# Optimization experiments

Hardware: AMD Instinct MI355X
Metric: run time of the kernel (lower is better)

The kernel has to match this reference:

```python
import jax, jax.numpy as jnp
import numpy as np

D_MODEL = 1024
N_HEADS = 16
DK = D_MODEL // N_HEADS


def setup_inputs() -> dict:
    key = jax.random.key(0)
    k1, k2, k3, k4 = jax.random.split(key, 4)
    x = jax.random.normal(k1, (2, 2048, D_MODEL), dtype=jnp.float32)
    # torch nn.Linear stores weight as [out_features, in_features]
    W_qkv = jax.random.normal(k2, (3 * D_MODEL, D_MODEL), dtype=jnp.float32) * (1.0 / np.sqrt(D_MODEL))
    W_proj = jax.random.normal(k3, (D_MODEL, D_MODEL), dtype=jnp.float32) * (1.0 / np.sqrt(D_MODEL))
    b_proj = jax.random.normal(k4, (D_MODEL,), dtype=jnp.float32) * 0.01
    return {"x": x, "W_qkv": W_qkv, "W_proj": W_proj, "b_proj": b_proj}


def reference(x, W_qkv, W_proj, b_proj):
    B, L, D = x.shape
    qkv = x @ W_qkv.T                      # [B, L, 3D]
    q, k, v = jnp.split(qkv, 3, axis=-1)   # each [B, L, D]

    def split_heads(t):
        return t.reshape(B, L, N_HEADS, DK).transpose(0, 2, 1, 3)  # [B, H, L, dk]

    q, k, v = map(split_heads, (q, k, v))
    scale = jnp.float32(1.0 / np.sqrt(DK))
    scores = jnp.einsum('bhid,bhjd->bhij', q, k) * scale  # [B, H, L, L]
    attn = jax.nn.softmax(scores, axis=-1)
    out = jnp.einsum('bhij,bhjd->bhid', attn, v)           # [B, H, L, dk]
    out = out.transpose(0, 2, 1, 3).reshape(B, L, D)
    return out @ W_proj.T + b_proj
```

## Files before the change

kernel.cpp:

```cpp
#include <hip/hip_runtime.h>
#include <stdint.h>

typedef unsigned short ushort_t;
typedef __bf16 bf16x4 __attribute__((ext_vector_type(4)));
typedef __bf16 bf16x8 __attribute__((ext_vector_type(8)));
typedef float f32x4 __attribute__((ext_vector_type(4)));
typedef float f32x16 __attribute__((ext_vector_type(16)));
typedef unsigned short us8 __attribute__((ext_vector_type(8)));
typedef unsigned short us4v __attribute__((ext_vector_type(4)));

__device__ __forceinline__ float bf2f(ushort_t u) {
  union { uint32_t u; float f; } v; v.u = ((uint32_t)u) << 16; return v.f;
}
__device__ __forceinline__ ushort_t f2bf(float f) {
  union { float f; uint32_t u; } v; v.f = f;
  uint32_t u = v.u;
  uint32_t r = (u + 0x7FFFu + ((u >> 16) & 1u)) >> 16;
  return (ushort_t)r;
}
__device__ __forceinline__ uint32_t pkbf(float a, float b) {
  __bf16 x = (__bf16)a, y = (__bf16)b;
  uint32_t ux = __builtin_bit_cast(unsigned short, x);
  uint32_t uy = __builtin_bit_cast(unsigned short, y);
  return ux | (uy << 16);
}
__device__ __forceinline__ void gload_lds16(const void* g, void* l) {
  __builtin_amdgcn_global_load_lds(
      (const __attribute__((address_space(1))) void*)g,
      (__attribute__((address_space(3))) void*)l, 16, 0, 0);
}
__device__ __forceinline__ void tr2(const ushort_t* p, bf16x4& lo, bf16x4& hi) {
  asm volatile("ds_read_b64_tr_b16 %0, %2\n\t"
               "ds_read_b64_tr_b16 %1, %2 offset:128"
               : "=&v"(lo), "=&v"(hi)
               : "v"((const __attribute__((address_space(3))) ushort_t*)p));
}

template <typename T> __device__ __forceinline__ T to_out(float f);
template <> __device__ __forceinline__ ushort_t to_out<ushort_t>(float f) { return f2bf(f); }
template <> __device__ __forceinline__ float to_out<float>(float f) { return f; }

__global__ void f2b_kernel(const float* __restrict__ in, ushort_t* __restrict__ out, int n4) {
  int i = blockIdx.x * blockDim.x + threadIdx.x;
  int stride = gridDim.x * blockDim.x;
  for (; i < n4; i += stride) {
    float4 v = ((const float4*)in)[i];
    us4v o;
    o[0] = f2bf(v.x); o[1] = f2bf(v.y); o[2] = f2bf(v.z); o[3] = f2bf(v.w);
    ((us4v*)out)[i] = o;
  }
}

template<bool BIAS, typename OT>
__global__ __launch_bounds__(256, 2) void gemm_bt(
    const ushort_t* __restrict__ A, const ushort_t* __restrict__ W,
    const float* __restrict__ bias, OT* __restrict__ C,
    int M, int N, int K)
{
  __shared__ ushort_t As[128 * 64];
  __shared__ ushort_t Bs[128 * 64];
  const int t = threadIdx.x;
  const int w = t >> 6, lane = t & 63;
  const int lg = lane >> 4, lc = lane & 15;
  const int rowbase = blockIdx.y * 128;
  const int colbase = blockIdx.x * 128;
  const int wr = (w >> 1) * 64, wc = (w & 1) * 64;

  f32x4 acc[4][4] = {};
  const int nkt = K >> 6;

  for (int kt = 0; kt < nkt; ++kt) {
#pragma unroll
    for (int i = 0; i < 4; ++i) {
      int off = (i * 256 + t) * 16;
      int row = off >> 7;
      int cb  = off & 127;
      int ec  = cb ^ ((row & 7) << 4);
      gload_lds16(A + (size_t)(rowbase + row) * K + kt * 64 + (ec >> 1),
                  (char*)As + off);
      gload_lds16(W + (size_t)(colbase + row) * K + kt * 64 + (ec >> 1),
                  (char*)Bs + off);
    }
    __syncthreads();
#pragma unroll
    for (int kk = 0; kk < 2; ++kk) {
      bf16x8 af[4], bf[4];
#pragma unroll
      for (int m = 0; m < 4; ++m) {
        int row = wr + m * 16 + lc;
        int kb  = (lg * 16 + kk * 64) ^ ((row & 7) << 4);
        af[m] = *(const bf16x8*)((const char*)As + row * 128 + kb);
        int col = wc + m * 16 + lc;
        int kb2 = (lg * 16 + kk * 64) ^ ((col & 7) << 4);
        bf[m] = *(const bf16x8*)((const char*)Bs + col * 128 + kb2);
      }
#pragma unroll
      for (int m = 0; m < 4; ++m)
#pragma unroll
        for (int n = 0; n < 4; ++n)
          acc[m][n] = __builtin_amdgcn_mfma_f32_16x16x32_bf16(af[m], bf[n],
                                                              acc[m][n], 0, 0, 0);
    }
    __syncthreads();
  }

#pragma unroll
  for (int m = 0; m < 4; ++m) {
    int r0 = rowbase + wr + m * 16 + lg * 4;
#pragma unroll
    for (int n = 0; n < 4; ++n) {
      int c0 = colbase + wc + n * 16 + lc;
      float bv = 0.f;
      if (BIAS) bv = bias[c0];
#pragma unroll
      for (int j = 0; j < 4; ++j)
        C[(size_t)(r0 + j) * N + c0] = to_out<OT>(acc[m][n][j] + bv);
    }
  }
}

__global__ __launch_bounds__(256, 2) void attn_fwd(
    const ushort_t* __restrict__ qkv, ushort_t* __restrict__ aout)
{
  __shared__ ushort_t Ks[2][64 * 64];
  __shared__ ushort_t Vs[2][64 * 64];

  const int t = threadIdx.x, w = t >> 6, lane = t & 63;
  const int l31 = lane & 31, hi = lane >> 5;
  const int lc = lane & 15;

  const int d = blockIdx.x;
  const int qt = (d >> 3) & 15;
  const int bh = (d & 7) * 4 + (d >> 7);
  const int b = bh >> 4, h = bh & 15;

  const ushort_t* Qg = qkv + (size_t)(b * 2048) * 3072 + h * 64;
  const ushort_t* Kg = Qg + 1024;
  const ushort_t* Vg = Qg + 2048;

  auto stage_k = [&](ushort_t* Kd, int kt) {
#pragma unroll
    for (int i = 0; i < 2; ++i) {
      int off = (i * 256 + t) * 16;
      int row = off >> 7;
      int cb  = off & 127;
      int ec  = cb ^ ((row & 7) << 4);
      gload_lds16(Kg + (size_t)(kt * 64 + row) * 3072 + (ec >> 1),
                  (char*)Kd + off);
    }
  };
  int vr[2], vc0[2], vdst[2];
#pragma unroll
  for (int i = 0; i < 2; ++i) {
    int u = i * 256 + t;
    vr[i]  = u >> 3;
    vc0[i] = (u & 7) * 8;
    vdst[i] = (vc0[i] >> 4) * 2048 + (vr[i] >> 2) * 128 + (vr[i] & 3) * 32 +
              (vc0[i] & 8) * 2;
  }

  const ushort_t* qrow_p = Qg + (size_t)(qt * 128 + w * 32 + l31) * 3072;
  bf16x8 qf[4];
#pragma unroll
  for (int kk = 0; kk < 4; ++kk)
    qf[kk] = *(const bf16x8*)(qrow_p + kk * 16 + hi * 8);

  stage_k(Ks[0], 0);
#pragma unroll
  for (int i = 0; i < 2; ++i) {
    us8 v = *(const us8*)(Vg + (size_t)vr[i] * 3072 + vc0[i]);
    *(us8*)((char*)Vs[0] + vdst[i]) = v;
  }
  __syncthreads();

  f32x16 oacc0 = {}, oacc1 = {};
  float m = -1e30f, l = 0.f;
  const float SC = 0.125f * 1.44269504088896f;

  int cur = 0;
  for (int kt = 0; kt < 32; ++kt) {
    us8 vnext[2];
    if (kt < 31) {
      stage_k(Ks[cur ^ 1], kt + 1);
#pragma unroll
      for (int i = 0; i < 2; ++i)
        vnext[i] = *(const us8*)(Vg + (size_t)((kt + 1) * 64 + vr[i]) * 3072 + vc0[i]);
    }

    const ushort_t* Kc = Ks[cur];
    f32x16 s0 = {}, s1 = {};
#pragma unroll
    for (int kk = 0; kk < 4; ++kk) {
      int cbyte = (kk * 32 + hi * 16);
      int r0 = l31, r1 = 32 + l31;
      bf16x8 kf0 = *(const bf16x8*)((const char*)Kc + r0 * 128 +
                                    (cbyte ^ ((r0 & 7) << 4)));
      bf16x8 kf1 = *(const bf16x8*)((const char*)Kc + r1 * 128 +
                                    (cbyte ^ ((r1 & 7) << 4)));
      s0 = __builtin_amdgcn_mfma_f32_32x32x16_bf16(kf0, qf[kk], s0, 0, 0, 0);
      s1 = __builtin_amdgcn_mfma_f32_32x32x16_bf16(kf1, qf[kk], s1, 0, 0, 0);
    }

    float tm = fmaxf(s0[0], s1[0]);
#pragma unroll
    for (int i = 1; i < 16; ++i) tm = fmaxf(tm, fmaxf(s0[i], s1[i]));
    tm = fmaxf(tm, __shfl_xor(tm, 32));
    float tms = tm * SC;
    if (__any(tms > m + 8.f)) {
      float nm = fmaxf(m, tms);
      float so = __builtin_amdgcn_exp2f(m - nm);
      m = nm; l *= so;
#pragma unroll
      for (int r = 0; r < 16; ++r) {
        float sor = __shfl(so, (r & 3) + 8 * (r >> 2) + 4 * hi);
        oacc0[r] *= sor; oacc1[r] *= sor;
      }
    }
#pragma unroll
    for (int i = 0; i < 16; ++i) {
      s0[i] = __builtin_amdgcn_exp2f(__builtin_fmaf(s0[i], SC, -m));
      s1[i] = __builtin_amdgcn_exp2f(__builtin_fmaf(s1[i], SC, -m));
    }
    float rs = 0.f;
#pragma unroll
    for (int i = 0; i < 16; ++i) rs += s0[i] + s1[i];
    rs += __shfl_xor(rs, 32);
    l += rs;

    uint32_t pk0[8], pk1[8];
#pragma unroll
    for (int j = 0; j < 8; ++j) {
      pk0[j] = pkbf(s0[2 * j], s0[2 * j + 1]);
      pk1[j] = pkbf(s1[2 * j], s1[2 * j + 1]);
    }

    if (kt < 31) {
#pragma unroll
      for (int i = 0; i < 2; ++i)
        *(us8*)((char*)Vs[cur ^ 1] + vdst[i]) = vnext[i];
    }

    const ushort_t* Vc = Vs[cur];
    bf16x8 pa[4], vf[4][2];
#pragma unroll
    for (int ks = 0; ks < 4; ++ks) {
      int j0 = 4 * (ks & 1);
      uint32_t x0 = (ks < 2) ? pk0[j0]     : pk1[j0];
      uint32_t x1 = (ks < 2) ? pk0[j0 + 1] : pk1[j0 + 1];
      uint32_t y0 = (ks < 2) ? pk0[j0 + 2] : pk1[j0 + 2];
      uint32_t y1 = (ks < 2) ? pk0[j0 + 3] : pk1[j0 + 3];
      asm volatile("v_permlane32_swap_b32 %0, %1" : "+v"(x0), "+v"(y0));
      asm volatile("v_permlane32_swap_b32 %0, %1" : "+v"(x1), "+v"(y1));
      union { uint32_t du[4]; bf16x8 v; } U;
      U.du[0] = x0; U.du[1] = x1; U.du[2] = y0; U.du[3] = y1;
      pa[ks] = U.v;
      const int m16 = (lane >> 4) & 1;
#pragma unroll
      for (int nd = 0; nd < 2; ++nd) {
        bf16x4 lo, hh;
        tr2(Vc + (nd * 2 + m16) * 1024 + (4 * ks + 2 * hi) * 64 + lc * 4, lo, hh);
        vf[ks][nd] = __builtin_shufflevector(lo, hh, 0, 1, 2, 3, 4, 5, 6, 7);
      }
    }
    asm volatile("s_waitcnt lgkmcnt(0)" ::: "memory");
    __builtin_amdgcn_sched_barrier(0);
#pragma unroll
    for (int ks = 0; ks < 4; ++ks) {
      oacc0 = __builtin_amdgcn_mfma_f32_32x32x16_bf16(pa[ks], vf[ks][0], oacc0, 0, 0, 0);
      oacc1 = __builtin_amdgcn_mfma_f32_32x32x16_bf16(pa[ks], vf[ks][1], oacc1, 0, 0, 0);
    }

    __syncthreads();
    cur ^= 1;
  }

  float inv = 1.f / l;
#pragma unroll
  for (int r = 0; r < 16; ++r) {
    int crow = (r & 3) + 8 * (r >> 2) + 4 * hi;
    float iq = __shfl(inv, crow);
    int qrow = qt * 128 + w * 32 + crow;
    size_t base = ((size_t)(b * 2048 + qrow)) * 1024 + h * 64 + l31;
    aout[base]      = f2bf(oacc0[r] * iq);
    aout[base + 32] = f2bf(oacc1[r] * iq);
  }
}

extern "C" void kernel_launch(void* const* d_in, const int* in_sizes, int n_in,
                              void* d_out, int out_size, void* d_ws, size_t ws_size,
                              hipStream_t stream) {
  const float* x     = (const float*)d_in[0];
  const float* Wqkv  = (const float*)d_in[1];
  const float* Wproj = (const float*)d_in[2];
  const float* bproj = (const float*)d_in[3];
  float* out = (float*)d_out;

  ushort_t* qkv   = (ushort_t*)d_ws;
  ushort_t* aout  = qkv   + (size_t)4096 * 3072;
  ushort_t* xb    = aout  + (size_t)4096 * 1024;
  ushort_t* wqb   = xb    + (size_t)4096 * 1024;
  ushort_t* wpb   = wqb   + (size_t)3072 * 1024;

  dim3 blk(256);
  f2b_kernel<<<1024, blk, 0, stream>>>(x,     xb,  4096 * 1024 / 4);
  f2b_kernel<<<1024, blk, 0, stream>>>(Wqkv,  wqb, 3072 * 1024 / 4);
  f2b_kernel<<<512,  blk, 0, stream>>>(Wproj, wpb, 1024 * 1024 / 4);

  gemm_bt<false, ushort_t><<<dim3(24, 32), blk, 0, stream>>>(
      xb, wqb, nullptr, qkv, 4096, 3072, 1024);
  attn_fwd<<<dim3(512), blk, 0, stream>>>(qkv, aout);
  gemm_bt<true, float><<<dim3(8, 32), blk, 0, stream>>>(
      aout, wpb, bproj, out, 4096, 1024, 1024);
}
```

Baseline: 125.7 us.

## Load K tiles directly into registers instead of staging through LDS

Each wave now loads its K fragments straight from global memory into double-buffered register arrays (kA/kB) and prefetches the next tile, rather than staging K through swizzled shared memory with async LDS loads. The loop is unrolled by two so the K and V buffers alternate without an index variable, and the max reduction is rewritten as a linear chain. This removes the LDS traffic and LDS footprint for K. In exchange, each of the four waves fetches the same K rows from global memory or cache, and the extra 16 bf16x8 registers may push up register pressure under the 2-blocks-per-CU launch bound.

```diff
diff --git a/kernel.cpp b/kernel.cpp
--- a/kernel.cpp
+++ b/kernel.cpp
@@ -122,7 +122,6 @@
 __global__ __launch_bounds__(256, 2) void attn_fwd(
     const ushort_t* __restrict__ qkv, ushort_t* __restrict__ aout)
 {
-  __shared__ ushort_t Ks[2][64 * 64];
   __shared__ ushort_t Vs[2][64 * 64];
 
   const int t = threadIdx.x, w = t >> 6, lane = t & 63;
@@ -138,17 +137,6 @@
   const ushort_t* Kg = Qg + 1024;
   const ushort_t* Vg = Qg + 2048;
 
-  auto stage_k = [&](ushort_t* Kd, int kt) {
-#pragma unroll
-    for (int i = 0; i < 2; ++i) {
-      int off = (i * 256 + t) * 16;
-      int row = off >> 7;
-      int cb  = off & 127;
-      int ec  = cb ^ ((row & 7) << 4);
-      gload_lds16(Kg + (size_t)(kt * 64 + row) * 3072 + (ec >> 1),
-                  (char*)Kd + off);
-    }
-  };
   int vr[2], vc0[2], vdst[2];
 #pragma unroll
   for (int i = 0; i < 2; ++i) {
@@ -165,7 +153,15 @@
   for (int kk = 0; kk < 4; ++kk)
     qf[kk] = *(const bf16x8*)(qrow_p + kk * 16 + hi * 8);
 
-  stage_k(Ks[0], 0);
+  const ushort_t* krow0 = Kg + (size_t)l31 * 3072 + hi * 8;
+  const ushort_t* krow1 = Kg + (size_t)(32 + l31) * 3072 + hi * 8;
+
+  bf16x8 kA[8], kB[8];
+#pragma unroll
+  for (int kk = 0; kk < 4; ++kk) {
+    kA[2 * kk]     = *(const bf16x8*)(krow0 + kk * 16);
+    kA[2 * kk + 1] = *(const bf16x8*)(krow1 + kk * 16);
+  }
 #pragma unroll
   for (int i = 0; i < 2; ++i) {
     us8 v = *(const us8*)(Vg + (size_t)vr[i] * 3072 + vc0[i]);
@@ -176,103 +172,118 @@
   f32x16 oacc0 = {}, oacc1 = {};
   float m = -1e30f, l = 0.f;
   const float SC = 0.125f * 1.44269504088896f;
-
-  int cur = 0;
-  for (int kt = 0; kt < 32; ++kt) {
-    us8 vnext[2];
-    if (kt < 31) {
-      stage_k(Ks[cur ^ 1], kt + 1);
-#pragma unroll
-      for (int i = 0; i < 2; ++i)
-        vnext[i] = *(const us8*)(Vg + (size_t)((kt + 1) * 64 + vr[i]) * 3072 + vc0[i]);
-    }
-
-    const ushort_t* Kc = Ks[cur];
-    f32x16 s0 = {}, s1 = {};
-#pragma unroll
-    for (int kk = 0; kk < 4; ++kk) {
-      int cbyte = (kk * 32 + hi * 16);
-      int r0 = l31, r1 = 32 + l31;
-      bf16x8 kf0 = *(const bf16x8*)((const char*)Kc + r0 * 128 +
-                                    (cbyte ^ ((r0 & 7) << 4)));
-      bf16x8 kf1 = *(const bf16x8*)((const char*)Kc + r1 * 128 +
-                                    (cbyte ^ ((r1 & 7) << 4)));
-      s0 = __builtin_amdgcn_mfma_f32_32x32x16_bf16(kf0, qf[kk], s0, 0, 0, 0);
-      s1 = __builtin_amdgcn_mfma_f32_32x32x16_bf16(kf1, qf[kk], s1, 0, 0, 0);
-    }
-
-    float tm = fmaxf(s0[0], s1[0]);
-#pragma unroll
-    for (int i = 1; i < 16; ++i) tm = fmaxf(tm, fmaxf(s0[i], s1[i]));
-    tm = fmaxf(tm, __shfl_xor(tm, 32));
-    float tms = tm * SC;
-    if (__any(tms > m + 8.f)) {
-      float nm = fmaxf(m, tms);
-      float so = __builtin_amdgcn_exp2f(m - nm);
-      m = nm; l *= so;
-#pragma unroll
-      for (int r = 0; r < 16; ++r) {
-        float sor = __shfl(so, (r & 3) + 8 * (r >> 2) + 4 * hi);
-        oacc0[r] *= sor; oacc1[r] *= sor;
-      }
-    }
-#pragma unroll
-    for (int i = 0; i < 16; ++i) {
-      s0[i] = __builtin_amdgcn_exp2f(__builtin_fmaf(s0[i], SC, -m));
-      s1[i] = __builtin_amdgcn_exp2f(__builtin_fmaf(s1[i], SC, -m));
-    }
-    float rs = 0.f;
-#pragma unroll
-    for (int i = 0; i < 16; ++i) rs += s0[i] + s1[i];
-    rs += __shfl_xor(rs, 32);
-    l += rs;
-
-    uint32_t pk0[8], pk1[8];
-#pragma unroll
-    for (int j = 0; j < 8; ++j) {
-      pk0[j] = pkbf(s0[2 * j], s0[2 * j + 1]);
-      pk1[j] = pkbf(s1[2 * j], s1[2 * j + 1]);
-    }
-
-    if (kt < 31) {
-#pragma unroll
-      for (int i = 0; i < 2; ++i)
-        *(us8*)((char*)Vs[cur ^ 1] + vdst[i]) = vnext[i];
-    }
-
-    const ushort_t* Vc = Vs[cur];
-    bf16x8 pa[4], vf[4][2];
-#pragma unroll
-    for (int ks = 0; ks < 4; ++ks) {
-      int j0 = 4 * (ks & 1);
-      uint32_t x0 = (ks < 2) ? pk0[j0]     : pk1[j0];
-      uint32_t x1 = (ks < 2) ? pk0[j0 + 1] : pk1[j0 + 1];
-      uint32_t y0 = (ks < 2) ? pk0[j0 + 2] : pk1[j0 + 2];
-      uint32_t y1 = (ks < 2) ? pk0[j0 + 3] : pk1[j0 + 3];
-      asm volatile("v_permlane32_swap_b32 %0, %1" : "+v"(x0), "+v"(y0));
-      asm volatile("v_permlane32_swap_b32 %0, %1" : "+v"(x1), "+v"(y1));
-      union { uint32_t du[4]; bf16x8 v; } U;
-      U.du[0] = x0; U.du[1] = x1; U.du[2] = y0; U.du[3] = y1;
-      pa[ks] = U.v;
-      const int m16 = (lane >> 4) & 1;
-#pragma unroll
-      for (int nd = 0; nd < 2; ++nd) {
-        bf16x4 lo, hh;
-        tr2(Vc + (nd * 2 + m16) * 1024 + (4 * ks + 2 * hi) * 64 + lc * 4, lo, hh);
-        vf[ks][nd] = __builtin_shufflevector(lo, hh, 0, 1, 2, 3, 4, 5, 6, 7);
-      }
-    }
-    asm volatile("s_waitcnt lgkmcnt(0)" ::: "memory");
-    __builtin_amdgcn_sched_barrier(0);
-#pragma unroll
-    for (int ks = 0; ks < 4; ++ks) {
-      oacc0 = __builtin_amdgcn_mfma_f32_32x32x16_bf16(pa[ks], vf[ks][0], oacc0, 0, 0, 0);
-      oacc1 = __builtin_amdgcn_mfma_f32_32x32x16_bf16(pa[ks], vf[ks][1], oacc1, 0, 0, 0);
-    }
-
-    __syncthreads();
-    cur ^= 1;
-  }
+  const int m16 = (lane >> 4) & 1;
+
+#define ATTN_ITER(KT, KUSE, KPRE, VCUR, VNXT)                                  \
+  {                                                                            \
+    const int kt_ = (KT);                                                      \
+    us8 vnx0, vnx1;                                                            \
+    if (kt_ < 31) {             \
+      _Pragma("unroll")                                                        \
+      for (int kk = 0; kk < 4; ++kk) {                                         \
+        KPRE[2 * kk]     = *(const bf16x8*)(krow0 + (size_t)(kt_ + 1) * 196608 \
+                                            + kk * 16);                        \
+        KPRE[2 * kk + 1] = *(const bf16x8*)(krow1 + (size_t)(kt_ + 1) * 196608 \
+                                            + kk * 16);                        \
+      }                                                                        \
+      vnx0 = *(const us8*)(Vg + (size_t)((kt_ + 1) * 64 + vr[0]) * 3072 + vc0[0]); \
+      vnx1 = *(const us8*)(Vg + (size_t)((kt_ + 1) * 64 + vr[1]) * 3072 + vc0[1]); \
+    }                                                                          \
+                                                            \
+    f32x16 s0 = {}, s1 = {};                                                   \
+    _Pragma("unroll")                                                          \
+    for (int kk = 0; kk < 4; ++kk) {                                           \
+      s0 = __builtin_amdgcn_mfma_f32_32x32x16_bf16(KUSE[2 * kk],     qf[kk], s0, 0, 0, 0); \
+      s1 = __builtin_amdgcn_mfma_f32_32x32x16_bf16(KUSE[2 * kk + 1], qf[kk], s1, 0, 0, 0); \
+    }                                                                          \
+              \
+    float tm = fmaxf(fmaxf(s0[0], s0[1]), s0[2]);                              \
+    tm = fmaxf(fmaxf(tm, s0[3]), s0[4]);                                       \
+    tm = fmaxf(fmaxf(tm, s0[5]), s0[6]);                                       \
+    tm = fmaxf(fmaxf(tm, s0[7]), s0[8]);                                       \
+    tm = fmaxf(fmaxf(tm, s0[9]), s0[10]);                                      \
+    tm = fmaxf(fmaxf(tm, s0[11]), s0[12]);                                     \
+    tm = fmaxf(fmaxf(tm, s0[13]), s0[14]);                                     \
+    tm = fmaxf(fmaxf(tm, s0[15]), s1[0]);                                      \
+    tm = fmaxf(fmaxf(tm, s1[1]), s1[2]);                                       \
+    tm = fmaxf(fmaxf(tm, s1[3]), s1[4]);                                       \
+    tm = fmaxf(fmaxf(tm, s1[5]), s1[6]);                                       \
+    tm = fmaxf(fmaxf(tm, s1[7]), s1[8]);                                       \
+    tm = fmaxf(fmaxf(tm, s1[9]), s1[10]);                                      \
+    tm = fmaxf(fmaxf(tm, s1[11]), s1[12]);                                     \
+    tm = fmaxf(fmaxf(tm, s1[13]), s1[14]);                                     \
+    tm = fmaxf(tm, s1[15]);                                                    \
+    tm = fmaxf(tm, __shfl_xor(tm, 32));                                        \
+    float tms = tm * SC;                                                       \
+    if (__any(tms > m + 8.f)) {              \
+      float nm = fmaxf(m, tms);                                                \
+      float so = __builtin_amdgcn_exp2f(m - nm);                               \
+      m = nm; l *= so;                                                         \
+      _Pragma("unroll")                                                        \
+      for (int r = 0; r < 16; ++r) {                                           \
+        float sor = __shfl(so, (r & 3) + 8 * (r >> 2) + 4 * hi);               \
+        oacc0[r] *= sor; oacc1[r] *= sor;                                      \
+      }                                                                        \
+    }                                                                          \
+    _Pragma("unroll")                                                          \
+    for (int i = 0; i < 16; ++i) {                                             \
+      s0[i] = __builtin_amdgcn_exp2f(__builtin_fmaf(s0[i], SC, -m));           \
+      s1[i] = __builtin_amdgcn_exp2f(__builtin_fmaf(s1[i], SC, -m));           \
+    }                                                                          \
+    float rs = 0.f;                                                            \
+    _Pragma("unroll")                                                          \
+    for (int i = 0; i < 16; ++i) rs += s0[i] + s1[i];                          \
+    rs += __shfl_xor(rs, 32);                                                  \
+    l += rs;                                                                   \
+                                                         \
+    uint32_t pk0[8], pk1[8];                                                   \
+    _Pragma("unroll")                                                          \
+    for (int j = 0; j < 8; ++j) {                                              \
+      pk0[j] = pkbf(s0[2 * j], s0[2 * j + 1]);                                 \
+      pk1[j] = pkbf(s1[2 * j], s1[2 * j + 1]);                                 \
+    }                                                                          \
+                   \
+    if (kt_ < 31) {                                                            \
+      *(us8*)((char*)(VNXT) + vdst[0]) = vnx0;                                 \
+      *(us8*)((char*)(VNXT) + vdst[1]) = vnx1;                                 \
+    }                                                                          \
+                      \
+    bf16x8 pa[4], vf[4][2];                                                    \
+    _Pragma("unroll")                                                          \
+    for (int ks = 0; ks < 4; ++ks) {                                           \
+      int j0 = 4 * (ks & 1);                                                   \
+      uint32_t x0 = (ks < 2) ? pk0[j0]     : pk1[j0];                          \
+      uint32_t x1 = (ks < 2) ? pk0[j0 + 1] : pk1[j0 + 1];                      \
+      uint32_t y0 = (ks < 2) ? pk0[j0 + 2] : pk1[j0 + 2];                      \
+      uint32_t y1 = (ks < 2) ? pk0[j0 + 3] : pk1[j0 + 3];                      \
+      asm volatile("v_permlane32_swap_b32 %0, %1" : "+v"(x0), "+v"(y0));       \
+      asm volatile("v_permlane32_swap_b32 %0, %1" : "+v"(x1), "+v"(y1));       \
+      union { uint32_t du[4]; bf16x8 v; } U;                                   \
+      U.du[0] = x0; U.du[1] = x1; U.du[2] = y0; U.du[3] = y1;                  \
+      pa[ks] = U.v;                                                            \
+      _Pragma("unroll")                                                        \
+      for (int nd = 0; nd < 2; ++nd) {                                         \
+        bf16x4 lo, hh;                                                         \
+        tr2((VCUR) + (nd * 2 + m16) * 1024 + (4 * ks + 2 * hi) * 64 + lc * 4,  \
+            lo, hh);                                                           \
+        vf[ks][nd] = __builtin_shufflevector(lo, hh, 0, 1, 2, 3, 4, 5, 6, 7);  \
+      }                                                                        \
+    }                                                                          \
+    asm volatile("s_waitcnt lgkmcnt(0)" ::: "memory");           \
+    __builtin_amdgcn_sched_barrier(0);                                         \
+    _Pragma("unroll")                                                          \
+    for (int ks = 0; ks < 4; ++ks) {                                           \
+      oacc0 = __builtin_amdgcn_mfma_f32_32x32x16_bf16(pa[ks], vf[ks][0], oacc0, 0, 0, 0); \
+      oacc1 = __builtin_amdgcn_mfma_f32_32x32x16_bf16(pa[ks], vf[ks][1], oacc1, 0, 0, 0); \
+    }                                                                          \
+    __syncthreads();                                                           \
+  }
+
+  for (int kt2 = 0; kt2 < 16; ++kt2) {
+    ATTN_ITER(2 * kt2,     kA, kB, Vs[0], Vs[1])
+    ATTN_ITER(2 * kt2 + 1, kB, kA, Vs[1], Vs[0])
+  }
+#undef ATTN_ITER
 
   float inv = 1.f / l;
 #pragma unroll
```

New measurement: 132.9 us. 1.06x slower.

## Split attention over KV halves with merge kernel, fuse casts, set MFMA priority

Applied to the files above, without the earlier changes.

Attention now splits the key/value sequence into two halves, launching twice as many blocks. Each block writes an unnormalized partial output plus its running max and sum, and a new merge kernel combines the two halves with softmax rescaling. The aim is more parallelism across the GPU, since 512 blocks underfill it. The cost is an extra kernel launch, extra memory traffic, and bf16 rounding of the partial outputs. It also fuses the three fp32-to-bf16 conversion launches into one and raises wave priority around the MFMA sections.

```diff
diff --git a/kernel.cpp b/kernel.cpp
--- a/kernel.cpp
+++ b/kernel.cpp
@@ -40,14 +40,21 @@
 template <> __device__ __forceinline__ ushort_t to_out<ushort_t>(float f) { return f2bf(f); }
 template <> __device__ __forceinline__ float to_out<float>(float f) { return f; }
 
-__global__ void f2b_kernel(const float* __restrict__ in, ushort_t* __restrict__ out, int n4) {
+__global__ void f2b3_kernel(const float* __restrict__ a, ushort_t* __restrict__ ao, int na,
+                            const float* __restrict__ b, ushort_t* __restrict__ bo, int nb,
+                            const float* __restrict__ c, ushort_t* __restrict__ co, int nc) {
   int i = blockIdx.x * blockDim.x + threadIdx.x;
+  int total = na + nb + nc;
   int stride = gridDim.x * blockDim.x;
-  for (; i < n4; i += stride) {
-    float4 v = ((const float4*)in)[i];
+  for (; i < total; i += stride) {
+    const float* src; ushort_t* dst; int j = i;
+    if (j < na) { src = a; dst = ao; }
+    else if ((j -= na) < nb) { src = b; dst = bo; }
+    else { j -= nb; src = c; dst = co; }
+    float4 v = ((const float4*)src)[j];
     us4v o;
     o[0] = f2bf(v.x); o[1] = f2bf(v.y); o[2] = f2bf(v.z); o[3] = f2bf(v.w);
-    ((us4v*)out)[i] = o;
+    ((us4v*)dst)[j] = o;
   }
 }
 
@@ -120,7 +127,8 @@
 }
 
 __global__ __launch_bounds__(256, 2) void attn_fwd(
-    const ushort_t* __restrict__ qkv, ushort_t* __restrict__ aout)
+    const ushort_t* __restrict__ qkv, ushort_t* __restrict__ o1,
+    ushort_t* __restrict__ o2, float2* __restrict__ ml)
 {
   __shared__ ushort_t Ks[2][64 * 64];
   __shared__ ushort_t Vs[2][64 * 64];
@@ -131,12 +139,13 @@
 
   const int d = blockIdx.x;
   const int qt = (d >> 3) & 15;
-  const int bh = (d & 7) * 4 + (d >> 7);
+  const int split = (d >> 7) & 1;
+  const int bh = (d & 7) * 4 + ((d >> 8) & 3);
   const int b = bh >> 4, h = bh & 15;
 
   const ushort_t* Qg = qkv + (size_t)(b * 2048) * 3072 + h * 64;
-  const ushort_t* Kg = Qg + 1024;
-  const ushort_t* Vg = Qg + 2048;
+  const ushort_t* Kg = Qg + 1024 + (size_t)split * 1024 * 3072;
+  const ushort_t* Vg = Qg + 2048 + (size_t)split * 1024 * 3072;
 
   auto stage_k = [&](ushort_t* Kd, int kt) {
 #pragma unroll
@@ -176,11 +185,12 @@
   f32x16 oacc0 = {}, oacc1 = {};
   float m = -1e30f, l = 0.f;
   const float SC = 0.125f * 1.44269504088896f;
+  const int m16 = (lane >> 4) & 1;
 
   int cur = 0;
-  for (int kt = 0; kt < 32; ++kt) {
+  for (int kt = 0; kt < 16; ++kt) {
     us8 vnext[2];
-    if (kt < 31) {
+    if (kt < 15) {
       stage_k(Ks[cur ^ 1], kt + 1);
 #pragma unroll
       for (int i = 0; i < 2; ++i)
@@ -189,6 +199,7 @@
 
     const ushort_t* Kc = Ks[cur];
     f32x16 s0 = {}, s1 = {};
+    __builtin_amdgcn_s_setprio(1);
 #pragma unroll
     for (int kk = 0; kk < 4; ++kk) {
       int cbyte = (kk * 32 + hi * 16);
@@ -200,6 +211,7 @@
       s0 = __builtin_amdgcn_mfma_f32_32x32x16_bf16(kf0, qf[kk], s0, 0, 0, 0);
       s1 = __builtin_amdgcn_mfma_f32_32x32x16_bf16(kf1, qf[kk], s1, 0, 0, 0);
     }
+    __builtin_amdgcn_s_setprio(0);
 
     float tm = fmaxf(s0[0], s1[0]);
 #pragma unroll
@@ -234,7 +246,7 @@
       pk1[j] = pkbf(s1[2 * j], s1[2 * j + 1]);
     }
 
-    if (kt < 31) {
+    if (kt < 15) {
 #pragma unroll
       for (int i = 0; i < 2; ++i)
         *(us8*)((char*)Vs[cur ^ 1] + vdst[i]) = vnext[i];
@@ -254,7 +266,6 @@
       union { uint32_t du[4]; bf16x8 v; } U;
       U.du[0] = x0; U.du[1] = x1; U.du[2] = y0; U.du[3] = y1;
       pa[ks] = U.v;
-      const int m16 = (lane >> 4) & 1;
 #pragma unroll
       for (int nd = 0; nd < 2; ++nd) {
         bf16x4 lo, hh;
@@ -264,26 +275,55 @@
     }
     asm volatile("s_waitcnt lgkmcnt(0)" ::: "memory");
     __builtin_amdgcn_sched_barrier(0);
+    __builtin_amdgcn_s_setprio(1);
 #pragma unroll
     for (int ks = 0; ks < 4; ++ks) {
       oacc0 = __builtin_amdgcn_mfma_f32_32x32x16_bf16(pa[ks], vf[ks][0], oacc0, 0, 0, 0);
       oacc1 = __builtin_amdgcn_mfma_f32_32x32x16_bf16(pa[ks], vf[ks][1], oacc1, 0, 0, 0);
     }
+    __builtin_amdgcn_s_setprio(0);
 
     __syncthreads();
     cur ^= 1;
   }
 
-  float inv = 1.f / l;
+  ushort_t* op = split ? o2 : o1;
 #pragma unroll
   for (int r = 0; r < 16; ++r) {
     int crow = (r & 3) + 8 * (r >> 2) + 4 * hi;
-    float iq = __shfl(inv, crow);
     int qrow = qt * 128 + w * 32 + crow;
     size_t base = ((size_t)(b * 2048 + qrow)) * 1024 + h * 64 + l31;
-    aout[base]      = f2bf(oacc0[r] * iq);
-    aout[base + 32] = f2bf(oacc1[r] * iq);
-  }
+    op[base]      = f2bf(oacc0[r]);
+    op[base + 32] = f2bf(oacc1[r]);
+  }
+  if (hi == 0) {
+    int qrow = qt * 128 + w * 32 + l31;
+    float2 v; v.x = m; v.y = l;
+    ml[(size_t)split * 65536 + (size_t)(b * 2048 + qrow) * 16 + h] = v;
+  }
+}
+
+__global__ void merge_kernel(ushort_t* __restrict__ o1,
+                             const ushort_t* __restrict__ o2,
+                             const float2* __restrict__ ml) {
+  int i = blockIdx.x * blockDim.x + threadIdx.x;
+  int row = i >> 7;
+  int col = (i & 127) * 8;
+  int h = col >> 6;
+  float2 a = ml[(size_t)row * 16 + h];
+  float2 c = ml[65536 + (size_t)row * 16 + h];
+  float M = fmaxf(a.x, c.x);
+  float w1 = __builtin_amdgcn_exp2f(a.x - M);
+  float w2 = __builtin_amdgcn_exp2f(c.x - M);
+  float inv = 1.f / (w1 * a.y + w2 * c.y);
+  float s1 = w1 * inv, s2 = w2 * inv;
+  us8 v1 = ((const us8*)o1)[i];
+  us8 v2 = ((const us8*)o2)[i];
+  us8 o;
+#pragma unroll
+  for (int j = 0; j < 8; ++j)
+    o[j] = f2bf(bf2f(v1[j]) * s1 + bf2f(v2[j]) * s2);
+  ((us8*)o1)[i] = o;
 }
 
 extern "C" void kernel_launch(void* const* d_in, const int* in_sizes, int n_in,
@@ -300,15 +340,17 @@
   ushort_t* xb    = aout  + (size_t)4096 * 1024;
   ushort_t* wqb   = xb    + (size_t)4096 * 1024;
   ushort_t* wpb   = wqb   + (size_t)3072 * 1024;
+  float2*   mlbuf = (float2*)(wpb + (size_t)1024 * 1024);
 
   dim3 blk(256);
-  f2b_kernel<<<1024, blk, 0, stream>>>(x,     xb,  4096 * 1024 / 4);
-  f2b_kernel<<<1024, blk, 0, stream>>>(Wqkv,  wqb, 3072 * 1024 / 4);
-  f2b_kernel<<<512,  blk, 0, stream>>>(Wproj, wpb, 1024 * 1024 / 4);
+  f2b3_kernel<<<2048, blk, 0, stream>>>(x, xb, 4096 * 1024 / 4,
+                                        Wqkv, wqb, 3072 * 1024 / 4,
+                                        Wproj, wpb, 1024 * 1024 / 4);
 
   gemm_bt<false, ushort_t><<<dim3(24, 32), blk, 0, stream>>>(
       xb, wqb, nullptr, qkv, 4096, 3072, 1024);
-  attn_fwd<<<dim3(512), blk, 0, stream>>>(qkv, aout);
+  attn_fwd<<<dim3(1024), blk, 0, stream>>>(qkv, aout, xb, mlbuf);
+  merge_kernel<<<2048, blk, 0, stream>>>(aout, xb, mlbuf);
   gemm_bt<true, float><<<dim3(8, 32), blk, 0, stream>>>(
       aout, wpb, bproj, out, 4096, 1024, 1024);
 }
```

After: 127.0 us. No clear change (+1.0%).
